# Kernel tuning notes

Measured on AMD Instinct MI355X. Metric: run time of the kernel, lower is better.

Reference implementation:

```python
import jax, jax.numpy as jnp
import numpy as np

NUM_HEADS = 16

def setup_inputs() -> dict:
    key = jax.random.key(0)
    ks = jax.random.split(key, 8)
    B, S, X, D = 2, 2048, 1, 1024
    scale = 1.0 / np.sqrt(D)
    return {
        "query": jax.random.normal(ks[0], (B, S, X, D), jnp.float32),
        "key": jax.random.normal(ks[1], (B, S, X, D), jnp.float32),
        "value": jax.random.normal(ks[2], (B, S, X, D), jnp.float32),
        "Wq": jax.random.normal(ks[3], (D, D), jnp.float32) * scale,
        "bq": jnp.zeros((D,), jnp.float32),
        "Wk": jax.random.normal(ks[4], (D, D), jnp.float32) * scale,
        "bk": jnp.zeros((D,), jnp.float32),
        "Wv": jax.random.normal(ks[5], (D, D), jnp.float32) * scale,
        "bv": jnp.zeros((D,), jnp.float32),
        "Wo": jax.random.normal(ks[6], (D, D), jnp.float32) * scale,
        "bo": jnp.zeros((D,), jnp.float32),
    }

def _split_heads(x, B, H):
    # [B, S, X, D] -> [B, H, S*X, depth]
    D = x.shape[-1]
    return x.reshape(B, -1, H, D // H).transpose(0, 2, 1, 3)

def reference(query, key, value, Wq, bq, Wk, bk, Wv, bv, Wo, bo):
    B, S, X, D = query.shape
    H = NUM_HEADS
    q = _split_heads(query @ Wq + bq, B, H)   # [B,H,L,dh], L=S*X
    k = _split_heads(key @ Wk + bk, B, H)
    v = _split_heads(value @ Wv + bv, B, H)
    dh = k.shape[-1]
    logits = jnp.einsum("bhqd,bhkd->bhqk", q, k) / jnp.sqrt(jnp.float32(dh))
    attn = jax.nn.softmax(logits, axis=-1)
    out = jnp.einsum("bhqk,bhkd->bhqd", attn, v)   # [B,H,L,dh]
    out = out.transpose(0, 2, 1, 3).reshape(B, S, -1, D)  # [B,S,X,D]
    return out @ Wo + bo
```

## Files before the change

### kernel.cpp

```cpp
#include <hip/hip_runtime.h>
#include <cstdint>
#include <cstddef>

typedef __bf16 bf16x8 __attribute__((ext_vector_type(8)));
typedef float f32x4 __attribute__((ext_vector_type(4)));
typedef unsigned short u16;
typedef unsigned int u32;

static constexpr int Bn = 2;
static constexpr int L  = 2048;
static constexpr int Dm = 1024;
static constexpr int H  = 16;
static constexpr int DH = 64;
static constexpr int M  = Bn * L;

#define SC 0.18033688f

__device__ __forceinline__ u16 f2bf(float f) {
    union { float f; u32 u; } v; v.f = f;
    u32 u = v.u + 0x7FFFu + ((v.u >> 16) & 1u);
    return (u16)(u >> 16);
}

__device__ __forceinline__ void gl2lds16(const void* g, void* l) {
    __builtin_amdgcn_global_load_lds(
        (const __attribute__((address_space(1))) u32*)(uintptr_t)g,
        (__attribute__((address_space(3))) u32*)(uintptr_t)l, 16, 0, 0);
}

__global__ __launch_bounds__(256) void convert_in(
    const float* __restrict__ q, const float* __restrict__ k, const float* __restrict__ v,
    u16* __restrict__ dst)
{
    const float* src = (blockIdx.y == 0) ? q : (blockIdx.y == 1) ? k : v;
    u16* d = dst + (size_t)blockIdx.y * M * Dm;
    const size_t t = (size_t)blockIdx.x * 256 + threadIdx.x;
    const float4* s4 = reinterpret_cast<const float4*>(src) + t * 2;
    float4 f0 = s4[0], f1 = s4[1];
    u16 o[8] = { f2bf(f0.x), f2bf(f0.y), f2bf(f0.z), f2bf(f0.w),
                 f2bf(f1.x), f2bf(f1.y), f2bf(f1.z), f2bf(f1.w) };
    reinterpret_cast<uint4*>(d)[t] = *reinterpret_cast<uint4*>(o);
}

__global__ __launch_bounds__(256) void convert_wt(
    const float* __restrict__ Wq, const float* __restrict__ Wk,
    const float* __restrict__ Wv, const float* __restrict__ Wo,
    u16* __restrict__ dst)
{
    __shared__ u16 Ts[64][72];
    const int z = blockIdx.z;
    const float* W = (z == 0) ? Wq : (z == 1) ? Wk : (z == 2) ? Wv : Wo;
    u16* o = dst + (size_t)z * Dm * Dm;
    const int n0 = blockIdx.x * 64, k0 = blockIdx.y * 64;
    const int tid = threadIdx.x;

    {
        const int kr = tid >> 2, nc = (tid & 3) * 16;
        const float* s = W + (size_t)(k0 + kr) * Dm + n0 + nc;
        const float4* s4 = reinterpret_cast<const float4*>(s);
        float4 a = s4[0], b = s4[1], c = s4[2], d = s4[3];
        u16 t[16] = { f2bf(a.x), f2bf(a.y), f2bf(a.z), f2bf(a.w),
                      f2bf(b.x), f2bf(b.y), f2bf(b.z), f2bf(b.w),
                      f2bf(c.x), f2bf(c.y), f2bf(c.z), f2bf(c.w),
                      f2bf(d.x), f2bf(d.y), f2bf(d.z), f2bf(d.w) };
        *reinterpret_cast<uint4*>(&Ts[kr][nc])     = reinterpret_cast<uint4*>(t)[0];
        *reinterpret_cast<uint4*>(&Ts[kr][nc + 8]) = reinterpret_cast<uint4*>(t)[1];
    }
    __syncthreads();
    {
        const int nr = tid >> 2, kc = (tid & 3) * 16;
        u16 w[16];
        #pragma unroll
        for (int j = 0; j < 16; ++j) w[j] = Ts[kc + j][nr];
        u16* dptr = o + (size_t)(n0 + nr) * Dm + k0 + kc;
        *reinterpret_cast<uint4*>(dptr)     = reinterpret_cast<uint4*>(w)[0];
        *reinterpret_cast<uint4*>(dptr + 8) = reinterpret_cast<uint4*>(w)[1];
    }
}

__global__ __launch_bounds__(256) void gemm_qkv(
    const u16* __restrict__ Abuf, const u16* __restrict__ Wtb,
    const float* __restrict__ bq, const float* __restrict__ bk, const float* __restrict__ bv,
    u16* __restrict__ Qh, u16* __restrict__ Kh, u16* __restrict__ Vh)
{
    __shared__ u16 As[128 * 32];
    __shared__ u16 Bs[128 * 32];
    const int tid = threadIdx.x;
    const int wave = tid >> 6, lane = tid & 63;
    const int quad = lane >> 4, l16 = lane & 15;
    const int wr = wave >> 1, wc = wave & 1;
    const int z = blockIdx.z;
    const u16* A  = Abuf + (size_t)z * M * Dm;
    const u16* Bt = Wtb  + (size_t)z * Dm * Dm;
    const float* bias = (z == 0) ? bq : (z == 1) ? bk : bv;
    u16* out = (z == 0) ? Qh : (z == 1) ? Kh : Vh;
    const int n0 = blockIdx.x * 128, m0 = blockIdx.y * 128;

    const int srow = lane >> 2;
    const int skc  = (lane & 3) * 8;

    f32x4 acc[4][4] = {};

    for (int k0 = 0; k0 < Dm; k0 += 32) {
        __syncthreads();
        #pragma unroll
        for (int i = 0; i < 2; ++i) {
            const int ra = i * 64 + wave * 16;
            gl2lds16(A  + (size_t)(m0 + ra + srow) * Dm + k0 + skc, &As[ra * 32]);
            gl2lds16(Bt + (size_t)(n0 + ra + srow) * Dm + k0 + skc, &Bs[ra * 32]);
        }
        __syncthreads();
        bf16x8 af[4], bf[4];
        #pragma unroll
        for (int t = 0; t < 4; ++t) {
            af[t] = *reinterpret_cast<const bf16x8*>(&As[(wr * 64 + t * 16 + l16) * 32 + quad * 8]);
            bf[t] = *reinterpret_cast<const bf16x8*>(&Bs[(wc * 64 + t * 16 + l16) * 32 + quad * 8]);
        }
        #pragma unroll
        for (int mt = 0; mt < 4; ++mt)
            #pragma unroll
            for (int nt = 0; nt < 4; ++nt)
                acc[mt][nt] = __builtin_amdgcn_mfma_f32_16x16x32_bf16(af[mt], bf[nt], acc[mt][nt], 0, 0, 0);
    }

    const float qscale = (z == 0) ? SC : 1.0f;
    #pragma unroll
    for (int nt = 0; nt < 4; ++nt) {
        const int n = n0 + wc * 64 + nt * 16 + l16;
        const float badd = bias[n];
        const int h = n >> 6, d = n & 63;
        #pragma unroll
        for (int mt = 0; mt < 4; ++mt) {
            #pragma unroll
            for (int r = 0; r < 4; ++r) {
                const int m = m0 + wr * 64 + mt * 16 + quad * 4 + r;
                const int bb = m >> 11, ll = m & 2047;
                out[(((size_t)(bb * H + h)) * L + ll) * DH + d] = f2bf((acc[mt][nt][r] + badd) * qscale);
            }
        }
    }
}

__global__ __launch_bounds__(256) void transpose_v(
    const u16* __restrict__ Vh, u16* __restrict__ Vth)
{
    __shared__ u16 Ts[64][72];
    const int kt = blockIdx.x, h = blockIdx.y, b = blockIdx.z;
    const int tid = threadIdx.x;
    const size_t hb = ((size_t)(b * H + h)) * L * DH;

    {
        const int kr = tid >> 2, dc = (tid & 3) * 16;
        const u16* s = Vh + hb + (size_t)(kt * 64 + kr) * DH + dc;
        *reinterpret_cast<uint4*>(&Ts[kr][dc])     = *reinterpret_cast<const uint4*>(s);
        *reinterpret_cast<uint4*>(&Ts[kr][dc + 8]) = *reinterpret_cast<const uint4*>(s + 8);
    }
    __syncthreads();
    {
        const int dr = tid >> 2, kc = (tid & 3) * 16;
        u16 w[16];
        #pragma unroll
        for (int j = 0; j < 16; ++j) w[j] = Ts[kc + j][dr];
        u16* dptr = Vth + hb + (size_t)dr * L + kt * 64 + kc;
        *reinterpret_cast<uint4*>(dptr)     = reinterpret_cast<uint4*>(w)[0];
        *reinterpret_cast<uint4*>(dptr + 8) = reinterpret_cast<uint4*>(w)[1];
    }
}

__global__ __launch_bounds__(256) void attn(
    const u16* __restrict__ Qh, const u16* __restrict__ Kh,
    const u16* __restrict__ Vth, u16* __restrict__ ctx)
{
    __shared__ u16 Qs[64][72];
    __shared__ u16 Ks[64][72];
    __shared__ u16 Vts[64][72];
    __shared__ u16 Ps[4][16][72];

    const int tid = threadIdx.x;
    const int wave = tid >> 6, lane = tid & 63;
    const int quad = lane >> 4, l16 = lane & 15;
    const int qt = blockIdx.x, h = blockIdx.y, b = blockIdx.z;
    const size_t hb = ((size_t)(b * H + h)) * L * DH;

    const int srow = tid >> 2;
    const int scol = (tid & 3) * 16;

    {
        const u16* src = Qh + hb + (size_t)(qt * 64 + srow) * DH + scol;
        *reinterpret_cast<uint4*>(&Qs[srow][scol])     = *reinterpret_cast<const uint4*>(src);
        *reinterpret_cast<uint4*>(&Qs[srow][scol + 8]) = *reinterpret_cast<const uint4*>(src + 8);
    }
    __syncthreads();
    const bf16x8 aq0 = *reinterpret_cast<const bf16x8*>(&Qs[wave * 16 + l16][quad * 8]);
    const bf16x8 aq1 = *reinterpret_cast<const bf16x8*>(&Qs[wave * 16 + l16][32 + quad * 8]);

    float rsum[4] = {0.f, 0.f, 0.f, 0.f};
    f32x4 o_acc[4] = {};

    for (int kt = 0; kt < L / 64; ++kt) {
        __syncthreads();
        {
            const u16* src = Kh + hb + (size_t)(kt * 64 + srow) * DH + scol;
            *reinterpret_cast<uint4*>(&Ks[srow][scol])     = *reinterpret_cast<const uint4*>(src);
            *reinterpret_cast<uint4*>(&Ks[srow][scol + 8]) = *reinterpret_cast<const uint4*>(src + 8);
        }
        {
            const u16* src = Vth + hb + (size_t)srow * L + kt * 64 + scol;
            *reinterpret_cast<uint4*>(&Vts[srow][scol])     = *reinterpret_cast<const uint4*>(src);
            *reinterpret_cast<uint4*>(&Vts[srow][scol + 8]) = *reinterpret_cast<const uint4*>(src + 8);
        }
        __syncthreads();

        f32x4 s[4] = {};
        #pragma unroll
        for (int nt = 0; nt < 4; ++nt) {
            bf16x8 b0 = *reinterpret_cast<const bf16x8*>(&Ks[nt * 16 + l16][quad * 8]);
            bf16x8 b1 = *reinterpret_cast<const bf16x8*>(&Ks[nt * 16 + l16][32 + quad * 8]);
            s[nt] = __builtin_amdgcn_mfma_f32_16x16x32_bf16(aq0, b0, s[nt], 0, 0, 0);
            s[nt] = __builtin_amdgcn_mfma_f32_16x16x32_bf16(aq1, b1, s[nt], 0, 0, 0);
        }

        #pragma unroll
        for (int nt = 0; nt < 4; ++nt) {
            #pragma unroll
            for (int r = 0; r < 4; ++r) {
                const float p = __builtin_amdgcn_exp2f(s[nt][r]);
                rsum[r] += p;
                Ps[wave][quad * 4 + r][nt * 16 + l16] = f2bf(p);
            }
        }

        #pragma unroll
        for (int kc = 0; kc < 2; ++kc) {
            const bf16x8 ap = *reinterpret_cast<const bf16x8*>(&Ps[wave][l16][kc * 32 + quad * 8]);
            #pragma unroll
            for (int nt = 0; nt < 4; ++nt) {
                bf16x8 bv = *reinterpret_cast<const bf16x8*>(&Vts[nt * 16 + l16][kc * 32 + quad * 8]);
                o_acc[nt] = __builtin_amdgcn_mfma_f32_16x16x32_bf16(ap, bv, o_acc[nt], 0, 0, 0);
            }
        }
    }

    #pragma unroll
    for (int r = 0; r < 4; ++r) {
        float rs = rsum[r];
        rs += __shfl_xor(rs, 1);
        rs += __shfl_xor(rs, 2);
        rs += __shfl_xor(rs, 4);
        rs += __shfl_xor(rs, 8);
        const float inv = 1.0f / rs;
        const int qrow = qt * 64 + wave * 16 + quad * 4 + r;
        #pragma unroll
        for (int nt = 0; nt < 4; ++nt)
            ctx[((size_t)(b * L + qrow)) * Dm + h * DH + nt * 16 + l16] = f2bf(o_acc[nt][r] * inv);
    }
}

__global__ __launch_bounds__(256) void gemm_out(
    const u16* __restrict__ A, const u16* __restrict__ Bt,
    const float* __restrict__ bias, float* __restrict__ out)
{
    __shared__ u16 As[128 * 32];
    __shared__ u16 Bs[128 * 32];
    const int tid = threadIdx.x;
    const int wave = tid >> 6, lane = tid & 63;
    const int quad = lane >> 4, l16 = lane & 15;
    const int wr = wave >> 1, wc = wave & 1;
    const int n0 = blockIdx.x * 128, m0 = blockIdx.y * 128;

    const int srow = lane >> 2;
    const int skc  = (lane & 3) * 8;

    f32x4 acc[4][4] = {};

    for (int k0 = 0; k0 < Dm; k0 += 32) {
        __syncthreads();
        #pragma unroll
        for (int i = 0; i < 2; ++i) {
            const int ra = i * 64 + wave * 16;
            gl2lds16(A  + (size_t)(m0 + ra + srow) * Dm + k0 + skc, &As[ra * 32]);
            gl2lds16(Bt + (size_t)(n0 + ra + srow) * Dm + k0 + skc, &Bs[ra * 32]);
        }
        __syncthreads();
        bf16x8 af[4], bf[4];
        #pragma unroll
        for (int t = 0; t < 4; ++t) {
            af[t] = *reinterpret_cast<const bf16x8*>(&As[(wr * 64 + t * 16 + l16) * 32 + quad * 8]);
            bf[t] = *reinterpret_cast<const bf16x8*>(&Bs[(wc * 64 + t * 16 + l16) * 32 + quad * 8]);
        }
        #pragma unroll
        for (int mt = 0; mt < 4; ++mt)
            #pragma unroll
            for (int nt = 0; nt < 4; ++nt)
                acc[mt][nt] = __builtin_amdgcn_mfma_f32_16x16x32_bf16(af[mt], bf[nt], acc[mt][nt], 0, 0, 0);
    }

    #pragma unroll
    for (int nt = 0; nt < 4; ++nt) {
        const int n = n0 + wc * 64 + nt * 16 + l16;
        const float badd = bias[n];
        #pragma unroll
        for (int mt = 0; mt < 4; ++mt) {
            #pragma unroll
            for (int r = 0; r < 4; ++r) {
                const int m = m0 + wr * 64 + mt * 16 + quad * 4 + r;
                out[(size_t)m * Dm + n] = acc[mt][nt][r] + badd;
            }
        }
    }
}

extern "C" void kernel_launch(void* const* d_in, const int* in_sizes, int n_in,
                              void* d_out, int out_size, void* d_ws, size_t ws_size,
                              hipStream_t stream) {
    const float* q  = (const float*)d_in[0];
    const float* k  = (const float*)d_in[1];
    const float* v  = (const float*)d_in[2];
    const float* Wq = (const float*)d_in[3];
    const float* bq = (const float*)d_in[4];
    const float* Wk = (const float*)d_in[5];
    const float* bk = (const float*)d_in[6];
    const float* Wv = (const float*)d_in[7];
    const float* bv = (const float*)d_in[8];
    const float* Wo = (const float*)d_in[9];
    const float* bo = (const float*)d_in[10];
    float* out = (float*)d_out;

    const size_t per = (size_t)Bn * H * L * DH;
    u16* Abuf = (u16*)d_ws;
    u16* Wt   = Abuf + 3 * (size_t)M * Dm;
    u16* Qh   = Wt + 4 * (size_t)Dm * Dm;
    u16* Kh   = Qh + per;
    u16* Vh   = Kh + per;
    u16* Vth  = Vh + per;
    u16* ctx  = Abuf;

    convert_in <<<dim3((M * Dm) / 8 / 256, 3), 256, 0, stream>>>(q, k, v, Abuf);
    convert_wt <<<dim3(Dm / 64, Dm / 64, 4), 256, 0, stream>>>(Wq, Wk, Wv, Wo, Wt);
    gemm_qkv   <<<dim3(Dm / 128, M / 128, 3), 256, 0, stream>>>(Abuf, Wt, bq, bk, bv, Qh, Kh, Vh);
    transpose_v<<<dim3(L / 64, H, Bn), 256, 0, stream>>>(Vh, Vth);
    attn       <<<dim3(L / 64, H, Bn), 256, 0, stream>>>(Qh, Kh, Vth, ctx);
    gemm_out   <<<dim3(Dm / 128, M / 128), 256, 0, stream>>>(ctx, Wt + 3 * (size_t)Dm * Dm, bo, out);
}
```

Baseline: 258.8 us.

## Rewrite attention with 32x32 MFMA, register P, swizzled async LDS loads

The attention kernel now processes 128 queries per block, 32 per wave. It uses 32x32x16 MFMA with Q kept in registers and K/V tiles loaded asynchronously into XOR-swizzled LDS. The P matrix stays in registers through v_permlane32_swap instead of round-tripping through LDS, and output goes out via staged coalesced stores. The output GEMM tile is reduced to 128x64 to give more blocks. The aim is to cut LDS traffic, bank conflicts and instruction count in the attention loop. The cost is fewer attention blocks and more register pressure.

```diff
diff --git a/kernel.cpp b/kernel.cpp
--- a/kernel.cpp
+++ b/kernel.cpp
@@ -4,6 +4,7 @@
 
 typedef __bf16 bf16x8 __attribute__((ext_vector_type(8)));
 typedef float f32x4 __attribute__((ext_vector_type(4)));
+typedef float f32x16 __attribute__((ext_vector_type(16)));
 typedef unsigned short u16;
 typedef unsigned int u32;
 
@@ -171,125 +172,154 @@
     const u16* __restrict__ Qh, const u16* __restrict__ Kh,
     const u16* __restrict__ Vth, u16* __restrict__ ctx)
 {
-    __shared__ u16 Qs[64][72];
-    __shared__ u16 Ks[64][72];
-    __shared__ u16 Vts[64][72];
-    __shared__ u16 Ps[4][16][72];
-
+    __shared__ u16 KV[2 * 64 * 64];
+    __shared__ u16 Os[64 * 72];
+
+    const int tid  = threadIdx.x;
+    const int wave = tid >> 6, lane = tid & 63;
+    const int l31  = lane & 31, hh = lane >> 5;
+    const int qt = blockIdx.x, h = blockIdx.y, b = blockIdx.z;
+    const size_t hb = ((size_t)(b * H + h)) * L * DH;
+
+    const int q0 = qt * 128 + wave * 32;
+
+    bf16x8 qf[4];
+    {
+        const u16* qp = Qh + hb + (size_t)(q0 + l31) * DH + hh * 8;
+        #pragma unroll
+        for (int c = 0; c < 4; ++c)
+            qf[c] = *reinterpret_cast<const bf16x8*>(qp + c * 16);
+    }
+
+    const int r_off = lane >> 3;
+    const int s_sl  = lane & 7;
+
+    int vbK[2], vbV[2];
+    #pragma unroll
+    for (int t = 0; t < 2; ++t) {
+        const int rr = t * 32 + l31;
+        vbK[t] = rr * 128 + ((rr & 7) << 4);
+        vbV[t] = 2 * 64 * 64 + rr * 128 + ((rr & 7) << 4);
+    }
+    const char* ldsb = (const char*)KV;
+
+    float rsum = 0.f;
+    f32x16 oacc[2] = {};
+
+    for (int kt = 0; kt < L / 64; ++kt) {
+        __syncthreads();
+        #pragma unroll
+        for (int i = 0; i < 2; ++i) {
+            const int rr = wave * 16 + i * 8 + r_off;
+            gl2lds16(Kh  + hb + (size_t)(kt * 64 + rr) * DH + ((s_sl ^ (rr & 7)) << 3),
+                     (char*)KV + (wave * 16 + i * 8) * 128);
+            gl2lds16(Vth + hb + (size_t)rr * L + kt * 64 + ((s_sl ^ (rr & 7)) << 3),
+                     (char*)KV + 8192 + (wave * 16 + i * 8) * 128);
+        }
+        __syncthreads();
+
+        f32x16 st[2] = {};
+        #pragma unroll
+        for (int t = 0; t < 2; ++t) {
+            #pragma unroll
+            for (int c = 0; c < 4; ++c) {
+                bf16x8 kf = *reinterpret_cast<const bf16x8*>(ldsb + (vbK[t] ^ (((c << 1) | hh) << 4)));
+                st[t] = __builtin_amdgcn_mfma_f32_32x32x16_bf16(kf, qf[c], st[t], 0, 0, 0);
+            }
+        }
+
+        bf16x8 pfrag[4];
+        #pragma unroll
+        for (int t = 0; t < 2; ++t) {
+            float p[16];
+            #pragma unroll
+            for (int r = 0; r < 16; ++r) {
+                p[r] = __builtin_amdgcn_exp2f(st[t][r]);
+                rsum += p[r];
+            }
+            #pragma unroll
+            for (int g = 0; g < 2; ++g) {
+                float* pg = p + g * 8;
+                #pragma unroll
+                for (int j = 0; j < 4; ++j) {
+                    asm volatile("v_permlane32_swap_b32 %0, %1" : "+v"(pg[j]), "+v"(pg[j + 4]));
+                }
+                u16 pk[8];
+                #pragma unroll
+                for (int j = 0; j < 8; ++j) pk[j] = f2bf(pg[j]);
+                pfrag[t * 2 + g] = *reinterpret_cast<bf16x8*>(pk);
+            }
+        }
+
+        #pragma unroll
+        for (int t = 0; t < 2; ++t) {
+            #pragma unroll
+            for (int c = 0; c < 4; ++c) {
+                bf16x8 vf = *reinterpret_cast<const bf16x8*>(ldsb + (vbV[t] ^ (((c << 1) | hh) << 4)));
+                oacc[t] = __builtin_amdgcn_mfma_f32_32x32x16_bf16(vf, pfrag[c], oacc[t], 0, 0, 0);
+            }
+        }
+    }
+
+    rsum += __shfl_xor(rsum, 32);
+    const float inv = 1.0f / rsum;
+
+    for (int pass = 0; pass < 2; ++pass) {
+        __syncthreads();
+        if ((wave >> 1) == pass) {
+            const int qloc = (wave & 1) * 32 + l31;
+            #pragma unroll
+            for (int t = 0; t < 2; ++t)
+                #pragma unroll
+                for (int r = 0; r < 16; ++r) {
+                    const int d = t * 32 + (r & 3) + ((r >> 2) << 3) + hh * 4;
+                    Os[qloc * 72 + d] = f2bf(oacc[t][r] * inv);
+                }
+        }
+        __syncthreads();
+        {
+            const int row = tid >> 2, cc = (tid & 3) * 16;
+            u16* dst = ctx + ((size_t)(b * L + qt * 128 + pass * 64 + row)) * Dm + h * 64 + cc;
+            *reinterpret_cast<uint4*>(dst)     = *reinterpret_cast<const uint4*>(&Os[row * 72 + cc]);
+            *reinterpret_cast<uint4*>(dst + 8) = *reinterpret_cast<const uint4*>(&Os[row * 72 + cc + 8]);
+        }
+    }
+}
+
+__global__ __launch_bounds__(256) void gemm_out(
+    const u16* __restrict__ A, const u16* __restrict__ Bt,
+    const float* __restrict__ bias, float* __restrict__ out)
+{
+    __shared__ u16 As[128 * 32];
+    __shared__ u16 Bs[64 * 32];
     const int tid = threadIdx.x;
     const int wave = tid >> 6, lane = tid & 63;
     const int quad = lane >> 4, l16 = lane & 15;
-    const int qt = blockIdx.x, h = blockIdx.y, b = blockIdx.z;
-    const size_t hb = ((size_t)(b * H + h)) * L * DH;
-
-    const int srow = tid >> 2;
-    const int scol = (tid & 3) * 16;
-
-    {
-        const u16* src = Qh + hb + (size_t)(qt * 64 + srow) * DH + scol;
-        *reinterpret_cast<uint4*>(&Qs[srow][scol])     = *reinterpret_cast<const uint4*>(src);
-        *reinterpret_cast<uint4*>(&Qs[srow][scol + 8]) = *reinterpret_cast<const uint4*>(src + 8);
-    }
-    __syncthreads();
-    const bf16x8 aq0 = *reinterpret_cast<const bf16x8*>(&Qs[wave * 16 + l16][quad * 8]);
-    const bf16x8 aq1 = *reinterpret_cast<const bf16x8*>(&Qs[wave * 16 + l16][32 + quad * 8]);
-
-    float rsum[4] = {0.f, 0.f, 0.f, 0.f};
-    f32x4 o_acc[4] = {};
-
-    for (int kt = 0; kt < L / 64; ++kt) {
-        __syncthreads();
-        {
-            const u16* src = Kh + hb + (size_t)(kt * 64 + srow) * DH + scol;
-            *reinterpret_cast<uint4*>(&Ks[srow][scol])     = *reinterpret_cast<const uint4*>(src);
-            *reinterpret_cast<uint4*>(&Ks[srow][scol + 8]) = *reinterpret_cast<const uint4*>(src + 8);
-        }
-        {
-            const u16* src = Vth + hb + (size_t)srow * L + kt * 64 + scol;
-            *reinterpret_cast<uint4*>(&Vts[srow][scol])     = *reinterpret_cast<const uint4*>(src);
-            *reinterpret_cast<uint4*>(&Vts[srow][scol + 8]) = *reinterpret_cast<const uint4*>(src + 8);
-        }
-        __syncthreads();
-
-        f32x4 s[4] = {};
-        #pragma unroll
-        for (int nt = 0; nt < 4; ++nt) {
-            bf16x8 b0 = *reinterpret_cast<const bf16x8*>(&Ks[nt * 16 + l16][quad * 8]);
-            bf16x8 b1 = *reinterpret_cast<const bf16x8*>(&Ks[nt * 16 + l16][32 + quad * 8]);
-            s[nt] = __builtin_amdgcn_mfma_f32_16x16x32_bf16(aq0, b0, s[nt], 0, 0, 0);
-            s[nt] = __builtin_amdgcn_mfma_f32_16x16x32_bf16(aq1, b1, s[nt], 0, 0, 0);
-        }
-
-        #pragma unroll
-        for (int nt = 0; nt < 4; ++nt) {
-            #pragma unroll
-            for (int r = 0; r < 4; ++r) {
-                const float p = __builtin_amdgcn_exp2f(s[nt][r]);
-                rsum[r] += p;
-                Ps[wave][quad * 4 + r][nt * 16 + l16] = f2bf(p);
-            }
-        }
-
-        #pragma unroll
-        for (int kc = 0; kc < 2; ++kc) {
-            const bf16x8 ap = *reinterpret_cast<const bf16x8*>(&Ps[wave][l16][kc * 32 + quad * 8]);
-            #pragma unroll
-            for (int nt = 0; nt < 4; ++nt) {
-                bf16x8 bv = *reinterpret_cast<const bf16x8*>(&Vts[nt * 16 + l16][kc * 32 + quad * 8]);
-                o_acc[nt] = __builtin_amdgcn_mfma_f32_16x16x32_bf16(ap, bv, o_acc[nt], 0, 0, 0);
-            }
-        }
-    }
-
-    #pragma unroll
-    for (int r = 0; r < 4; ++r) {
-        float rs = rsum[r];
-        rs += __shfl_xor(rs, 1);
-        rs += __shfl_xor(rs, 2);
-        rs += __shfl_xor(rs, 4);
-        rs += __shfl_xor(rs, 8);
-        const float inv = 1.0f / rs;
-        const int qrow = qt * 64 + wave * 16 + quad * 4 + r;
-        #pragma unroll
-        for (int nt = 0; nt < 4; ++nt)
-            ctx[((size_t)(b * L + qrow)) * Dm + h * DH + nt * 16 + l16] = f2bf(o_acc[nt][r] * inv);
-    }
-}
-
-__global__ __launch_bounds__(256) void gemm_out(
-    const u16* __restrict__ A, const u16* __restrict__ Bt,
-    const float* __restrict__ bias, float* __restrict__ out)
-{
-    __shared__ u16 As[128 * 32];
-    __shared__ u16 Bs[128 * 32];
-    const int tid = threadIdx.x;
-    const int wave = tid >> 6, lane = tid & 63;
-    const int quad = lane >> 4, l16 = lane & 15;
-    const int wr = wave >> 1, wc = wave & 1;
-    const int n0 = blockIdx.x * 128, m0 = blockIdx.y * 128;
+    const int n0 = blockIdx.x * 64, m0 = blockIdx.y * 128;
 
     const int srow = lane >> 2;
     const int skc  = (lane & 3) * 8;
 
-    f32x4 acc[4][4] = {};
+    f32x4 acc[2][4] = {};
 
     for (int k0 = 0; k0 < Dm; k0 += 32) {
         __syncthreads();
         #pragma unroll
         for (int i = 0; i < 2; ++i) {
             const int ra = i * 64 + wave * 16;
-            gl2lds16(A  + (size_t)(m0 + ra + srow) * Dm + k0 + skc, &As[ra * 32]);
-            gl2lds16(Bt + (size_t)(n0 + ra + srow) * Dm + k0 + skc, &Bs[ra * 32]);
-        }
-        __syncthreads();
-        bf16x8 af[4], bf[4];
-        #pragma unroll
-        for (int t = 0; t < 4; ++t) {
-            af[t] = *reinterpret_cast<const bf16x8*>(&As[(wr * 64 + t * 16 + l16) * 32 + quad * 8]);
-            bf[t] = *reinterpret_cast<const bf16x8*>(&Bs[(wc * 64 + t * 16 + l16) * 32 + quad * 8]);
-        }
-        #pragma unroll
-        for (int mt = 0; mt < 4; ++mt)
+            gl2lds16(A + (size_t)(m0 + ra + srow) * Dm + k0 + skc, &As[ra * 32]);
+        }
+        gl2lds16(Bt + (size_t)(n0 + wave * 16 + srow) * Dm + k0 + skc, &Bs[wave * 16 * 32]);
+        __syncthreads();
+        bf16x8 af[2], bf[4];
+        #pragma unroll
+        for (int t = 0; t < 2; ++t)
+            af[t] = *reinterpret_cast<const bf16x8*>(&As[(wave * 32 + t * 16 + l16) * 32 + quad * 8]);
+        #pragma unroll
+        for (int t = 0; t < 4; ++t)
+            bf[t] = *reinterpret_cast<const bf16x8*>(&Bs[(t * 16 + l16) * 32 + quad * 8]);
+        #pragma unroll
+        for (int mt = 0; mt < 2; ++mt)
             #pragma unroll
             for (int nt = 0; nt < 4; ++nt)
                 acc[mt][nt] = __builtin_amdgcn_mfma_f32_16x16x32_bf16(af[mt], bf[nt], acc[mt][nt], 0, 0, 0);
@@ -297,13 +327,13 @@
 
     #pragma unroll
     for (int nt = 0; nt < 4; ++nt) {
-        const int n = n0 + wc * 64 + nt * 16 + l16;
+        const int n = n0 + nt * 16 + l16;
         const float badd = bias[n];
         #pragma unroll
-        for (int mt = 0; mt < 4; ++mt) {
+        for (int mt = 0; mt < 2; ++mt) {
             #pragma unroll
             for (int r = 0; r < 4; ++r) {
-                const int m = m0 + wr * 64 + mt * 16 + quad * 4 + r;
+                const int m = m0 + wave * 32 + mt * 16 + quad * 4 + r;
                 out[(size_t)m * Dm + n] = acc[mt][nt][r] + badd;
             }
         }
@@ -339,6 +369,6 @@
     convert_wt <<<dim3(Dm / 64, Dm / 64, 4), 256, 0, stream>>>(Wq, Wk, Wv, Wo, Wt);
     gemm_qkv   <<<dim3(Dm / 128, M / 128, 3), 256, 0, stream>>>(Abuf, Wt, bq, bk, bv, Qh, Kh, Vh);
     transpose_v<<<dim3(L / 64, H, Bn), 256, 0, stream>>>(Vh, Vth);
-    attn       <<<dim3(L / 64, H, Bn), 256, 0, stream>>>(Qh, Kh, Vth, ctx);
-    gemm_out   <<<dim3(Dm / 128, M / 128), 256, 0, stream>>>(ctx, Wt + 3 * (size_t)Dm * Dm, bo, out);
-}
+    attn       <<<dim3(L / 128, H, Bn), 256, 0, stream>>>(Qh, Kh, Vth, ctx);
+    gemm_out   <<<dim3(Dm / 64, M / 128), 256, 0, stream>>>(ctx, Wt + 3 * (size_t)Dm * Dm, bo, out);
+}
```

Measured after the change: 239.0 us. -7.6%, faster.
